# Optimization experiments

Hardware: AMD Instinct MI355X
Metric: run time of the kernel (lower is better)

Reference implementation:

```python
import jax, jax.numpy as jnp
import numpy as np

NU = 0.01 / np.pi  # Burgers viscosity
LAYERS = [2, 128, 128, 128, 128, 1]
N_EQ, N_INIT, N_BND = 131072, 4096, 4096


def setup_inputs() -> dict:
    key = jax.random.key(0)
    ks = jax.random.split(key, 16)
    inp = {
        'tx_equation': jax.random.uniform(ks[0], (N_EQ, 2), dtype=jnp.float32),
        'tx_init': jax.random.uniform(ks[1], (N_INIT, 2), dtype=jnp.float32),
        'tx_bound': jax.random.uniform(ks[2], (N_BND, 2), dtype=jnp.float32),
    }
    # Glorot-normal initialized Dense weights, zero biases (keras defaults in build_network)
    for i, (fin, fout) in enumerate(zip(LAYERS[:-1], LAYERS[1:])):
        std = np.sqrt(2.0 / (fin + fout)).astype(np.float32)
        inp[f'W{i}'] = jax.random.normal(ks[3 + i], (fin, fout), dtype=jnp.float32) * std
        inp[f'b{i}'] = jnp.zeros((fout,), dtype=jnp.float32)
    return inp


def _mlp_scalar(tx, Ws, bs):
    # tx: (2,) -> scalar u. tanh hidden layers, linear output.
    h = tx
    for W, b in zip(Ws[:-1], bs[:-1]):
        h = jnp.tanh(h @ W + b)
    return (h @ Ws[-1] + bs[-1])[0]


def reference(tx_equation, tx_init, tx_bound, W0, b0, W1, b1, W2, b2, W3, b3, W4, b4):
    Ws = [W0, W1, W2, W3, W4]
    bs = [b0, b1, b2, b3, b4]

    def u_s(tx):
        return _mlp_scalar(tx, Ws, bs)

    def u_x_s(tx):
        return jax.grad(u_s)(tx)[1]

    # PDE residual on collocation points
    u = jax.vmap(u_s)(tx_equation)                     # (N,)
    g = jax.vmap(jax.grad(u_s))(tx_equation)           # (N, 2) -> columns (u_t, u_x)
    u_t, u_x = g[:, 0], g[:, 1]
    u_xx = jax.vmap(jax.grad(u_x_s))(tx_equation)[:, 1]  # (N,)
    burgers_eq = (u_t + u * u_x - NU * u_xx)[:, None]     # (N, 1)

    # Initial / boundary predictions (single fused batch like tf.concat in call)
    tx_ib = jnp.concatenate([tx_init, tx_bound], axis=0)
    u_ib = jax.vmap(u_s)(tx_ib)[:, None]
    n_i = tx_init.shape[0]
    return burgers_eq, u_ib[:n_i], u_ib[n_i:]
```

## Files before the change

kernel.cpp:

```cpp
#include <hip/hip_runtime.h>
#include <math.h>

#define NU_F 0.0031830988618379067f
#define HS 136

typedef __attribute__((ext_vector_type(8))) _Float16 half8;
typedef __attribute__((ext_vector_type(4))) _Float16 half4;
typedef __attribute__((ext_vector_type(16))) float f32x16;

__device__ __forceinline__ float fast_tanh(float x) {
    const float e = __builtin_amdgcn_exp2f(x * 2.8853900817779268f);
    const float r = __builtin_amdgcn_rcpf(e + 1.f);
    return fmaf(-2.f, r, 1.f);
}

__global__ void prep_kernel(const float* __restrict__ W1,
                            const float* __restrict__ W2,
                            const float* __restrict__ W3,
                            _Float16* __restrict__ ws)
{
    const int g = blockIdx.x * 256 + threadIdx.x;
    const int l = g >> 14;
    const int r = g & 16383;
    const int n = r & 127;
    const int k = r >> 7;
    const float* W = (l == 0) ? W1 : (l == 1) ? W2 : W3;
    const float w = W[k * 128 + n];
    ws[l * 16384 + (k >> 4) * 2048 + n * 16 + (k & 15)] = (_Float16)w;
}

__launch_bounds__(256, 4)
__global__ void pinn_kernel(const float* __restrict__ tx_eq,
                            const float* __restrict__ tx_init,
                            const float* __restrict__ tx_bnd,
                            const float* __restrict__ W0, const float* __restrict__ b0,
                            const float* __restrict__ b1, const float* __restrict__ b2,
                            const float* __restrict__ b3,
                            const float* __restrict__ W4, const float* __restrict__ b4,
                            const _Float16* __restrict__ wt,
                            float* __restrict__ out)
{
    __shared__ _Float16 Hh[128][HS];

    const int tid   = threadIdx.x;
    const int blk   = blockIdx.x;
    const bool is_eq = (blk < 4096);
    const int w     = tid >> 6;
    const int lane  = tid & 63;
    const int col   = lane & 31;
    const int khalf = lane >> 5;
    const int ncol  = 32 * w + col;
    const int wofs  = ncol * 16 + khalf * 8;

    float tv, xv;
    if (is_eq) {
        const float2 t2 = ((const float2*)tx_eq)[blk * 32 + (tid >> 3)];
        tv = t2.x; xv = t2.y;
    } else {
        const int p  = tid >> 1;
        const int gp = (blk - 4096) * 128 + p;
        const float2* src = (gp < 4096) ? (const float2*)tx_init : (const float2*)tx_bnd;
        const int idx = (gp < 4096) ? gp : gp - 4096;
        const float2 t2 = src[idx];
        tv = t2.x; xv = t2.y;
    }

    const _Float16* ph = wt + wofs;
    half8 q0 = *(const half8*)(ph);
    half8 q1 = *(const half8*)(ph + 2048);
    half8 q2 = *(const half8*)(ph + 4096);
    half8 q3 = *(const half8*)(ph + 6144);
    half8 q4 = *(const half8*)(ph + 8192);
    half8 q5 = *(const half8*)(ph + 10240);
    half8 q6 = *(const half8*)(ph + 12288);
    half8 q7 = *(const half8*)(ph + 14336);

    f32x16 Z;
    #pragma unroll
    for (int e = 0; e < 16; ++e) Z[e] = 0.f;

    if (is_eq) {
        const int p  = tid >> 3;
        const int f0 = (tid & 7) * 16;
        const int m0 = 4 * p;
        #pragma unroll
        for (int half = 0; half < 2; ++half) {
            const int fb = f0 + 8 * half;
            float vch[4][8];
            #pragma unroll
            for (int j = 0; j < 8; ++j) {
                const int f = fb + j;
                const float w0v = W0[f];
                const float w1v = W0[128 + f];
                const float z = fmaf(tv, w0v, fmaf(xv, w1v, b0[f]));
                const float a = fast_tanh(z);
                const float s = 1.f - a * a;
                vch[0][j] = a;
                vch[1][j] = s * w0v;
                vch[2][j] = s * w1v;
                vch[3][j] = -2.f * a * s * w1v * w1v;
            }
            #pragma unroll
            for (int c = 0; c < 4; ++c) {
                half8 hh;
                #pragma unroll
                for (int j = 0; j < 8; ++j) hh[j] = (_Float16)vch[c][j];
                *(half8*)&Hh[m0 + c][fb] = hh;
            }
        }
    } else {
        const int p  = tid >> 1;
        const int f0 = (tid & 1) * 64;
        #pragma unroll
        for (int g = 0; g < 8; ++g) {
            half8 hh;
            #pragma unroll
            for (int j = 0; j < 8; ++j) {
                const int f = f0 + 8 * g + j;
                hh[j] = (_Float16)fast_tanh(fmaf(tv, W0[f], fmaf(xv, W0[128 + f], b0[f])));
            }
            *(half8*)&Hh[p][f0 + 8 * g] = hh;
        }
    }
    __syncthreads();

    const float* barr[3] = {b1, b2, b3};

    #pragma unroll 1
    for (int layer = 0; layer < 3; ++layer) {
        const float bias = barr[layer][ncol];

        f32x16 acc0, acc1, acc2, acc3;

#define KSTEP0(Q)                                                             \
        {                                                                     \
            const int k0 = khalf * 8;                                         \
            const half8 ah0 = *(const half8*)&Hh[col][k0];                    \
            const half8 ah1 = *(const half8*)&Hh[32 + col][k0];               \
            const half8 ah2 = *(const half8*)&Hh[64 + col][k0];               \
            const half8 ah3 = *(const half8*)&Hh[96 + col][k0];               \
            acc0 = __builtin_amdgcn_mfma_f32_32x32x16_f16(ah0, Q, Z, 0, 0, 0); \
            acc1 = __builtin_amdgcn_mfma_f32_32x32x16_f16(ah1, Q, Z, 0, 0, 0); \
            acc2 = __builtin_amdgcn_mfma_f32_32x32x16_f16(ah2, Q, Z, 0, 0, 0); \
            acc3 = __builtin_amdgcn_mfma_f32_32x32x16_f16(ah3, Q, Z, 0, 0, 0); \
        }
#define KSTEP(KT, Q)                                                          \
        {                                                                     \
            const int k0 = KT * 16 + khalf * 8;                               \
            const half8 ah0 = *(const half8*)&Hh[col][k0];                    \
            const half8 ah1 = *(const half8*)&Hh[32 + col][k0];               \
            const half8 ah2 = *(const half8*)&Hh[64 + col][k0];               \
            const half8 ah3 = *(const half8*)&Hh[96 + col][k0];               \
            acc0 = __builtin_amdgcn_mfma_f32_32x32x16_f16(ah0, Q, acc0, 0, 0, 0); \
            acc1 = __builtin_amdgcn_mfma_f32_32x32x16_f16(ah1, Q, acc1, 0, 0, 0); \
            acc2 = __builtin_amdgcn_mfma_f32_32x32x16_f16(ah2, Q, acc2, 0, 0, 0); \
            acc3 = __builtin_amdgcn_mfma_f32_32x32x16_f16(ah3, Q, acc3, 0, 0, 0); \
        }
        KSTEP0(q0) KSTEP(1, q1) KSTEP(2, q2) KSTEP(3, q3)
        KSTEP(4, q4) KSTEP(5, q5) KSTEP(6, q6) KSTEP(7, q7)
#undef KSTEP0
#undef KSTEP

        if (layer < 2) {
            ph += 16384;
            q0 = *(const half8*)(ph);
            q1 = *(const half8*)(ph + 2048);
            q2 = *(const half8*)(ph + 4096);
            q3 = *(const half8*)(ph + 6144);
            q4 = *(const half8*)(ph + 8192);
            q5 = *(const half8*)(ph + 10240);
            q6 = *(const half8*)(ph + 12288);
            q7 = *(const half8*)(ph + 14336);
        }

        half4 h16[4][4];
        #pragma unroll
        for (int mt = 0; mt < 4; ++mt)
            #pragma unroll
            for (int g = 0; g < 4; ++g) {
                const float A0 = (mt == 0 ? acc0 : mt == 1 ? acc1 : mt == 2 ? acc2 : acc3)[4 * g + 0];
                const float A1 = (mt == 0 ? acc0 : mt == 1 ? acc1 : mt == 2 ? acc2 : acc3)[4 * g + 1];
                const float A2 = (mt == 0 ? acc0 : mt == 1 ? acc1 : mt == 2 ? acc2 : acc3)[4 * g + 2];
                const float A3 = (mt == 0 ? acc0 : mt == 1 ? acc1 : mt == 2 ? acc2 : acc3)[4 * g + 3];
                half4 hv;
                if (is_eq) {
                    const float t = fast_tanh(A0 + bias);
                    const float s = 1.f - t * t;
                    hv[0] = (_Float16)t;
                    hv[1] = (_Float16)(s * A1);
                    hv[2] = (_Float16)(s * A2);
                    hv[3] = (_Float16)fmaf(s, A3, -2.f * t * s * A2 * A2);
                } else {
                    hv[0] = (_Float16)fast_tanh(A0 + bias);
                    hv[1] = (_Float16)fast_tanh(A1 + bias);
                    hv[2] = (_Float16)fast_tanh(A2 + bias);
                    hv[3] = (_Float16)fast_tanh(A3 + bias);
                }
                h16[mt][g] = hv;
            }

        __syncthreads();

        #pragma unroll
        for (int mt = 0; mt < 4; ++mt)
            #pragma unroll
            for (int g = 0; g < 4; ++g) {
                const int mrow0 = mt * 32 + 8 * g + 4 * khalf;
                Hh[mrow0 + 0][ncol] = h16[mt][g][0];
                Hh[mrow0 + 1][ncol] = h16[mt][g][1];
                Hh[mrow0 + 2][ncol] = h16[mt][g][2];
                Hh[mrow0 + 3][ncol] = h16[mt][g][3];
            }
        __syncthreads();
    }

    {
        const float b4v = b4[0];
        const int m = tid >> 1;
        const int q = tid & 1;
        float dot = 0.f;
        #pragma unroll
        for (int g = 0; g < 8; ++g) {
            const int f = 64 * q + 8 * g;
            const half8 hh = *(const half8*)&Hh[m][f];
            const float4 wa = *(const float4*)&W4[f];
            const float4 wb = *(const float4*)&W4[f + 4];
            dot = fmaf((float)hh[0], wa.x, dot);
            dot = fmaf((float)hh[1], wa.y, dot);
            dot = fmaf((float)hh[2], wa.z, dot);
            dot = fmaf((float)hh[3], wa.w, dot);
            dot = fmaf((float)hh[4], wb.x, dot);
            dot = fmaf((float)hh[5], wb.y, dot);
            dot = fmaf((float)hh[6], wb.z, dot);
            dot = fmaf((float)hh[7], wb.w, dot);
        }
        dot += __shfl_xor(dot, 1);

        if (is_eq) {
            const int base = (lane & 7) * 8;
            const float uu   = __shfl(dot, base + 0) + b4v;
            const float utv  = __shfl(dot, base + 2);
            const float uxv  = __shfl(dot, base + 4);
            const float uxxv = __shfl(dot, base + 6);
            if (lane < 8)
                out[blk * 32 + 8 * w + lane] = fmaf(uu, uxv, utv) - NU_F * uxxv;
        } else {
            if (q == 0)
                out[131072 + (blk - 4096) * 128 + m] = dot + b4v;
        }
    }
}

extern "C" void kernel_launch(void* const* d_in, const int* in_sizes, int n_in,
                              void* d_out, int out_size, void* d_ws, size_t ws_size,
                              hipStream_t stream)
{
    const float* tx_eq   = (const float*)d_in[0];
    const float* tx_init = (const float*)d_in[1];
    const float* tx_bnd  = (const float*)d_in[2];
    const float* W0 = (const float*)d_in[3];
    const float* b0 = (const float*)d_in[4];
    const float* W1 = (const float*)d_in[5];
    const float* b1 = (const float*)d_in[6];
    const float* W2 = (const float*)d_in[7];
    const float* b2 = (const float*)d_in[8];
    const float* W3 = (const float*)d_in[9];
    const float* b3 = (const float*)d_in[10];
    const float* W4 = (const float*)d_in[11];
    const float* b4 = (const float*)d_in[12];
    float* out = (float*)d_out;
    _Float16* wt = (_Float16*)d_ws;

    hipLaunchKernelGGL(prep_kernel, dim3(192), dim3(256), 0, stream, W1, W2, W3, wt);
    hipLaunchKernelGGL(pinn_kernel, dim3(4160), dim3(256), 0, stream,
                       tx_eq, tx_init, tx_bnd, W0, b0, b1, b2, b3, W4, b4,
                       (const _Float16*)wt, out);
}
```

Measured before the change: 163.2 us.

## Use 2x2 warp tiling for MFMA layers to halve LDS A-operand reads

Each wave's tile of the 128x128 hidden-layer GEMMs changes from one 32-column strip across all 128 rows to a 64x64 block. A fragments read from LDS are now reused across two B fragments held in registers, which halves LDS traffic per MFMA. In exchange each wave holds twice as many weight registers (16 half8 instead of 8), so launch bounds drop from 4 to 3 blocks per CU, lowering occupancy.

```diff
diff --git a/kernel.cpp b/kernel.cpp
--- a/kernel.cpp
+++ b/kernel.cpp
@@ -29,7 +29,7 @@
     ws[l * 16384 + (k >> 4) * 2048 + n * 16 + (k & 15)] = (_Float16)w;
 }
 
-__launch_bounds__(256, 4)
+__launch_bounds__(256, 3)
 __global__ void pinn_kernel(const float* __restrict__ tx_eq,
                             const float* __restrict__ tx_init,
                             const float* __restrict__ tx_bnd,
@@ -49,8 +49,10 @@
     const int lane  = tid & 63;
     const int col   = lane & 31;
     const int khalf = lane >> 5;
-    const int ncol  = 32 * w + col;
-    const int wofs  = ncol * 16 + khalf * 8;
+    const int wr    = w >> 1;
+    const int wc    = w & 1;
+    const int ncol0 = 64 * wc + col;
+    const int arow0 = 64 * wr + col;
 
     float tv, xv;
     if (is_eq) {
@@ -65,7 +67,7 @@
         tv = t2.x; xv = t2.y;
     }
 
-    const _Float16* ph = wt + wofs;
+    const _Float16* ph = wt + ncol0 * 16 + khalf * 8;
     half8 q0 = *(const half8*)(ph);
     half8 q1 = *(const half8*)(ph + 2048);
     half8 q2 = *(const half8*)(ph + 4096);
@@ -74,6 +76,14 @@
     half8 q5 = *(const half8*)(ph + 10240);
     half8 q6 = *(const half8*)(ph + 12288);
     half8 q7 = *(const half8*)(ph + 14336);
+    half8 r0 = *(const half8*)(ph + 512);
+    half8 r1 = *(const half8*)(ph + 512 + 2048);
+    half8 r2 = *(const half8*)(ph + 512 + 4096);
+    half8 r3 = *(const half8*)(ph + 512 + 6144);
+    half8 r4 = *(const half8*)(ph + 512 + 8192);
+    half8 r5 = *(const half8*)(ph + 512 + 10240);
+    half8 r6 = *(const half8*)(ph + 512 + 12288);
+    half8 r7 = *(const half8*)(ph + 512 + 14336);
 
     f32x16 Z;
     #pragma unroll
@@ -128,36 +138,33 @@
 
     #pragma unroll 1
     for (int layer = 0; layer < 3; ++layer) {
-        const float bias = barr[layer][ncol];
-
-        f32x16 acc0, acc1, acc2, acc3;
-
-#define KSTEP0(Q)                                                             \
+        const float bias0 = barr[layer][ncol0];
+        const float bias1 = barr[layer][ncol0 + 32];
+
+        f32x16 a00, a01, a10, a11;
+
+#define KSTEP0(Q, R)                                                          \
         {                                                                     \
             const int k0 = khalf * 8;                                         \
-            const half8 ah0 = *(const half8*)&Hh[col][k0];                    \
-            const half8 ah1 = *(const half8*)&Hh[32 + col][k0];               \
-            const half8 ah2 = *(const half8*)&Hh[64 + col][k0];               \
-            const half8 ah3 = *(const half8*)&Hh[96 + col][k0];               \
-            acc0 = __builtin_amdgcn_mfma_f32_32x32x16_f16(ah0, Q, Z, 0, 0, 0); \
-            acc1 = __builtin_amdgcn_mfma_f32_32x32x16_f16(ah1, Q, Z, 0, 0, 0); \
-            acc2 = __builtin_amdgcn_mfma_f32_32x32x16_f16(ah2, Q, Z, 0, 0, 0); \
-            acc3 = __builtin_amdgcn_mfma_f32_32x32x16_f16(ah3, Q, Z, 0, 0, 0); \
-        }
-#define KSTEP(KT, Q)                                                          \
+            const half8 ah0 = *(const half8*)&Hh[arow0][k0];                  \
+            const half8 ah1 = *(const half8*)&Hh[arow0 + 32][k0];             \
+            a00 = __builtin_amdgcn_mfma_f32_32x32x16_f16(ah0, Q, Z, 0, 0, 0); \
+            a01 = __builtin_amdgcn_mfma_f32_32x32x16_f16(ah0, R, Z, 0, 0, 0); \
+            a10 = __builtin_amdgcn_mfma_f32_32x32x16_f16(ah1, Q, Z, 0, 0, 0); \
+            a11 = __builtin_amdgcn_mfma_f32_32x32x16_f16(ah1, R, Z, 0, 0, 0); \
+        }
+#define KSTEP(KT, Q, R)                                                       \
         {                                                                     \
             const int k0 = KT * 16 + khalf * 8;                               \
-            const half8 ah0 = *(const half8*)&Hh[col][k0];                    \
-            const half8 ah1 = *(const half8*)&Hh[32 + col][k0];               \
-            const half8 ah2 = *(const half8*)&Hh[64 + col][k0];               \
-            const half8 ah3 = *(const half8*)&Hh[96 + col][k0];               \
-            acc0 = __builtin_amdgcn_mfma_f32_32x32x16_f16(ah0, Q, acc0, 0, 0, 0); \
-            acc1 = __builtin_amdgcn_mfma_f32_32x32x16_f16(ah1, Q, acc1, 0, 0, 0); \
-            acc2 = __builtin_amdgcn_mfma_f32_32x32x16_f16(ah2, Q, acc2, 0, 0, 0); \
-            acc3 = __builtin_amdgcn_mfma_f32_32x32x16_f16(ah3, Q, acc3, 0, 0, 0); \
-        }
-        KSTEP0(q0) KSTEP(1, q1) KSTEP(2, q2) KSTEP(3, q3)
-        KSTEP(4, q4) KSTEP(5, q5) KSTEP(6, q6) KSTEP(7, q7)
+            const half8 ah0 = *(const half8*)&Hh[arow0][k0];                  \
+            const half8 ah1 = *(const half8*)&Hh[arow0 + 32][k0];             \
+            a00 = __builtin_amdgcn_mfma_f32_32x32x16_f16(ah0, Q, a00, 0, 0, 0); \
+            a01 = __builtin_amdgcn_mfma_f32_32x32x16_f16(ah0, R, a01, 0, 0, 0); \
+            a10 = __builtin_amdgcn_mfma_f32_32x32x16_f16(ah1, Q, a10, 0, 0, 0); \
+            a11 = __builtin_amdgcn_mfma_f32_32x32x16_f16(ah1, R, a11, 0, 0, 0); \
+        }
+        KSTEP0(q0, r0) KSTEP(1, q1, r1) KSTEP(2, q2, r2) KSTEP(3, q3, r3)
+        KSTEP(4, q4, r4) KSTEP(5, q5, r5) KSTEP(6, q6, r6) KSTEP(7, q7, r7)
 #undef KSTEP0
 #undef KSTEP
 
@@ -171,45 +178,61 @@
             q5 = *(const half8*)(ph + 10240);
             q6 = *(const half8*)(ph + 12288);
             q7 = *(const half8*)(ph + 14336);
-        }
-
-        half4 h16[4][4];
-        #pragma unroll
-        for (int mt = 0; mt < 4; ++mt)
-            #pragma unroll
-            for (int g = 0; g < 4; ++g) {
-                const float A0 = (mt == 0 ? acc0 : mt == 1 ? acc1 : mt == 2 ? acc2 : acc3)[4 * g + 0];
-                const float A1 = (mt == 0 ? acc0 : mt == 1 ? acc1 : mt == 2 ? acc2 : acc3)[4 * g + 1];
-                const float A2 = (mt == 0 ? acc0 : mt == 1 ? acc1 : mt == 2 ? acc2 : acc3)[4 * g + 2];
-                const float A3 = (mt == 0 ? acc0 : mt == 1 ? acc1 : mt == 2 ? acc2 : acc3)[4 * g + 3];
-                half4 hv;
-                if (is_eq) {
-                    const float t = fast_tanh(A0 + bias);
-                    const float s = 1.f - t * t;
-                    hv[0] = (_Float16)t;
-                    hv[1] = (_Float16)(s * A1);
-                    hv[2] = (_Float16)(s * A2);
-                    hv[3] = (_Float16)fmaf(s, A3, -2.f * t * s * A2 * A2);
-                } else {
-                    hv[0] = (_Float16)fast_tanh(A0 + bias);
-                    hv[1] = (_Float16)fast_tanh(A1 + bias);
-                    hv[2] = (_Float16)fast_tanh(A2 + bias);
-                    hv[3] = (_Float16)fast_tanh(A3 + bias);
+            r0 = *(const half8*)(ph + 512);
+            r1 = *(const half8*)(ph + 512 + 2048);
+            r2 = *(const half8*)(ph + 512 + 4096);
+            r3 = *(const half8*)(ph + 512 + 6144);
+            r4 = *(const half8*)(ph + 512 + 8192);
+            r5 = *(const half8*)(ph + 512 + 10240);
+            r6 = *(const half8*)(ph + 512 + 12288);
+            r7 = *(const half8*)(ph + 512 + 14336);
+        }
+
+        half4 h16[2][2][4];
+        #pragma unroll
+        for (int mtl = 0; mtl < 2; ++mtl)
+            #pragma unroll
+            for (int nt = 0; nt < 2; ++nt) {
+                const float bias = nt ? bias1 : bias0;
+                #pragma unroll
+                for (int g = 0; g < 4; ++g) {
+                    const float A0 = (mtl == 0 ? (nt == 0 ? a00 : a01) : (nt == 0 ? a10 : a11))[4 * g + 0];
+                    const float A1 = (mtl == 0 ? (nt == 0 ? a00 : a01) : (nt == 0 ? a10 : a11))[4 * g + 1];
+                    const float A2 = (mtl == 0 ? (nt == 0 ? a00 : a01) : (nt == 0 ? a10 : a11))[4 * g + 2];
+                    const float A3 = (mtl == 0 ? (nt == 0 ? a00 : a01) : (nt == 0 ? a10 : a11))[4 * g + 3];
+                    half4 hv;
+                    if (is_eq) {
+                        const float t = fast_tanh(A0 + bias);
+                        const float s = 1.f - t * t;
+                        hv[0] = (_Float16)t;
+                        hv[1] = (_Float16)(s * A1);
+                        hv[2] = (_Float16)(s * A2);
+                        hv[3] = (_Float16)fmaf(s, A3, -2.f * t * s * A2 * A2);
+                    } else {
+                        hv[0] = (_Float16)fast_tanh(A0 + bias);
+                        hv[1] = (_Float16)fast_tanh(A1 + bias);
+                        hv[2] = (_Float16)fast_tanh(A2 + bias);
+                        hv[3] = (_Float16)fast_tanh(A3 + bias);
+                    }
+                    h16[mtl][nt][g] = hv;
                 }
-                h16[mt][g] = hv;
             }
 
         __syncthreads();
 
         #pragma unroll
-        for (int mt = 0; mt < 4; ++mt)
-            #pragma unroll
-            for (int g = 0; g < 4; ++g) {
-                const int mrow0 = mt * 32 + 8 * g + 4 * khalf;
-                Hh[mrow0 + 0][ncol] = h16[mt][g][0];
-                Hh[mrow0 + 1][ncol] = h16[mt][g][1];
-                Hh[mrow0 + 2][ncol] = h16[mt][g][2];
-                Hh[mrow0 + 3][ncol] = h16[mt][g][3];
+        for (int mtl = 0; mtl < 2; ++mtl)
+            #pragma unroll
+            for (int nt = 0; nt < 2; ++nt) {
+                const int nc = ncol0 + 32 * nt;
+                #pragma unroll
+                for (int g = 0; g < 4; ++g) {
+                    const int mrow0 = 64 * wr + 32 * mtl + 8 * g + 4 * khalf;
+                    Hh[mrow0 + 0][nc] = h16[mtl][nt][g][0];
+                    Hh[mrow0 + 1][nc] = h16[mtl][nt][g][1];
+                    Hh[mrow0 + 2][nc] = h16[mtl][nt][g][2];
+                    Hh[mrow0 + 3][nc] = h16[mtl][nt][g][3];
+                }
             }
         __syncthreads();
     }
```

New measurement: 168.7 us. 1.03x slower.
